# Kernel tuning notes

Measured on AMD Instinct MI355X. Metric: run time of the kernel, lower is better.

Reference implementation:

```python
import jax, jax.numpy as jnp
import numpy as np

S = 72
IMG_W, IMG_H = 640, 360
STRIDE = 32
FMAP_H, FMAP_W = IMG_H // STRIDE, IMG_W // STRIDE  # 11, 20
N_OFFSETS = S
N_STRIPS = S - 1
ANGLES = np.array([15.0, 22.0, 30.0, 39.0, 49.0, 60.0, 72.0, 80.0, 90.0, 100.0, 108.0, 120.0, 131.0, 141.0, 150.0, 158.0, 165.0])
N_ANG = 17
N_PRED = 2 + 2 + 1 + N_OFFSETS  # 77
N_EDGE = FMAP_W + 2 * FMAP_H    # 42
N_PROP = N_ANG * N_EDGE         # 714
NMS_THRES = 15.0
BACKBONE_C = 512
CONV_C = 1024


def _make_anchors():
    anchor_ys = np.linspace(1.0, 0.0, N_OFFSETS)
    tan = np.tan(np.deg2rad(ANGLES))
    def side(origins):
        out = np.zeros((N_ANG, N_PRED, len(origins)), np.float32)
        for i, (sx, sy) in enumerate(origins):
            out[:, 2, i] = 1.0 - sy
            out[:, 3, i] = sx
            out[:, 5:, i] = (sx + (sy - anchor_ys)[None, :] / tan[:, None]) * IMG_W
        return out.reshape(N_ANG * N_PRED, len(origins))
    left = side([(0.0, y) for y in np.linspace(1.0, 0.0, FMAP_H)])
    right = side([(1.0, y) for y in np.linspace(1.0, 0.0, FMAP_H)])
    bottom = side([(x, 1.0) for x in np.linspace(1.0, 0.0, FMAP_W)])
    anchors = np.zeros((N_ANG * N_PRED, FMAP_H, FMAP_W), np.float32)
    anchors[:, :, 0] = left
    anchors[:, :, -1] = right
    anchors[:, -1, :] = bottom
    edge = np.concatenate([anchors[:, :, 0], anchors[:, :, -1], anchors[:, -1, :]], 1)  # [1309,42]
    anch_dim = edge.reshape(N_ANG, N_PRED, N_EDGE).transpose(2, 0, 1).reshape(N_PROP, N_PRED)
    return jnp.asarray(anchors), jnp.asarray(anch_dim)


def setup_inputs():
    key = jax.random.key(0)
    ks = jax.random.split(key, 4)
    B = 32
    feat = jax.random.normal(ks[0], (B, BACKBONE_C, FMAP_H, FMAP_W), jnp.float32)
    W_conv = jax.random.normal(ks[1], (CONV_C, BACKBONE_C), jnp.float32) * 0.02
    b_conv = jnp.zeros((CONV_C,), jnp.float32)
    W_cls = jax.random.normal(ks[2], (2 * N_ANG, CONV_C), jnp.float32) * 0.02
    b_cls = jnp.zeros((2 * N_ANG,), jnp.float32)
    W_reg = jax.random.normal(ks[3], (N_ANG * (N_OFFSETS + 1), CONV_C), jnp.float32) * 0.02
    b_reg = jnp.zeros((N_ANG * (N_OFFSETS + 1),), jnp.float32)
    anchors, anchors_anchor_dim = _make_anchors()
    return {"feat": feat, "W_conv": W_conv, "b_conv": b_conv, "W_cls": W_cls, "b_cls": b_cls,
            "W_reg": W_reg, "b_reg": b_reg, "anchors": anchors, "anchors_anchor_dim": anchors_anchor_dim}


def _proposals(feat, W_conv, b_conv, W_cls, b_cls, W_reg, b_reg, anchors):
    B = feat.shape[0]
    features = jnp.einsum('bchw,oc->bohw', feat, W_conv) + b_conv[None, :, None, None]
    cls_f = jnp.einsum('bchw,oc->bohw', features, W_cls) + b_cls[None, :, None, None]
    reg_f = jnp.einsum('bchw,oc->bohw', features, W_reg) + b_reg[None, :, None, None]
    anch = anchors.reshape(N_ANG, N_PRED, FMAP_H, FMAP_W)
    cls_r = cls_f.reshape(B, N_ANG, 2, FMAP_H, FMAP_W)
    reg_r = reg_f.reshape(B, N_ANG, N_OFFSETS + 1, FMAP_H, FMAP_W)
    # slots 0:2 <- cls logits (set), slots 2:4 <- anchor (copied), slots 4: <- anchor + reg
    mid = jnp.broadcast_to(anch[None, :, 2:4], (B, N_ANG, 2, FMAP_H, FMAP_W))
    tail = anch[None, :, 4:] + reg_r
    lane = jnp.concatenate([cls_r, mid, tail], axis=2)  # [B,17,77,h,w]
    # gather the three feature-map edges: left col, right col, bottom row
    edges = jnp.concatenate([lane[:, :, :, :, 0], lane[:, :, :, :, -1], lane[:, :, :, -1, :]], axis=3)  # [B,17,77,42]
    return edges.transpose(0, 3, 1, 2).reshape(B, N_PROP, N_PRED)  # [B,714,77]


def _nms_one(props, scores):
    # greedy line-NMS over proposals of one image, shapes static
    order = jnp.argsort(-scores)
    p = props[order]
    start = jnp.clip(jnp.round(p[:, 2] * N_STRIPS), 0.0, float(N_STRIPS))
    end = jnp.clip(start + p[:, 4] - 1.0, 0.0, float(N_STRIPS))
    xs = p[:, 5:]  # [N,72]
    s = jnp.maximum(start[:, None], start[None, :])
    e = jnp.minimum(end[:, None], end[None, :])
    idx = jnp.arange(N_OFFSETS, dtype=p.dtype)
    m = (idx[None, None, :] >= s[..., None]) & (idx[None, None, :] <= e[..., None])  # [N,N,72]
    diff = jnp.abs(xs[:, None, :] - xs[None, :, :])  # [N,N,72]
    cnt = e - s + 1.0
    dist = jnp.where(cnt > 0, jnp.sum(diff * m, -1) / jnp.maximum(cnt, 1.0), jnp.inf)
    sup = dist < NMS_THRES
    n = p.shape[0]
    pos = jnp.arange(n)
    def step(suppressed, i):
        keep_i = ~suppressed[i]
        suppressed = suppressed | (keep_i & sup[i] & (pos > i))
        return suppressed, keep_i
    _, keep_sorted = jax.lax.scan(step, jnp.zeros(n, bool), pos)
    return jnp.zeros(n, bool).at[order].set(keep_sorted)


def reference(feat, W_conv, b_conv, W_cls, b_cls, W_reg, b_reg, anchors, anchors_anchor_dim):
    proposals = _proposals(feat, W_conv, b_conv, W_cls, b_cls, W_reg, b_reg, anchors)
    scores = jax.nn.softmax(proposals[..., :2], axis=-1)[..., 1]  # [B,714]
    keep_mask = jax.lax.map(lambda pr: _nms_one(pr[0], pr[1]), (proposals, scores))  # [B,714]
    return proposals, keep_mask, scores
```

## Files before the change

kernel.cpp:

```cpp
#include <hip/hip_runtime.h>
#include <math.h>

#define NB     32
#define FH     11
#define FW     20
#define CIN    512
#define CMID   1024
#define NANG   17
#define NPREDD 77
#define NEDGE  42
#define NPROPP 714
#define NOFF   72
#define NCLS   34
#define NREGR  1241
#define N2PAD  1280
#define MTOT   1344
#define NSTRIPSF 71.0f
#define PADK   40

typedef unsigned long long u64;
typedef unsigned short ushortt;
typedef short s8v __attribute__((ext_vector_type(8)));
typedef float f4v __attribute__((ext_vector_type(4)));

__device__ inline ushortt f2bf(float f) {
    unsigned u = __float_as_uint(f);
    u += 0x7fffu + ((u >> 16) & 1u);
    return (ushortt)(u >> 16);
}
__device__ inline float bf2f(ushortt h) {
    return __uint_as_float(((unsigned)h) << 16);
}

__global__ __launch_bounds__(256) void k_gather_split(const float* __restrict__ feat,
                                                      ushortt* __restrict__ Ahi,
                                                      ushortt* __restrict__ Alo)
{
    int idx = blockIdx.x * 256 + threadIdx.x;
    int m = idx >> 9, c = idx & 511;
    int b = m / NEDGE, e = m - b * NEDGE;
    int h, w;
    if (e < FH)          { h = e;      w = 0;      }
    else if (e < 2 * FH) { h = e - FH; w = FW - 1; }
    else                 { h = FH - 1; w = e - 2 * FH; }
    float v = feat[((size_t)(b * CIN + c) * FH + h) * FW + w];
    ushortt hi = f2bf(v);
    Ahi[idx] = hi;
    Alo[idx] = f2bf(v - bf2f(hi));
}

__global__ __launch_bounds__(256) void k_gemm1m(const ushortt* __restrict__ Ahi,
                                                const ushortt* __restrict__ Alo,
                                                const float* __restrict__ W,
                                                const float* __restrict__ bias,
                                                ushortt* __restrict__ Chi,
                                                ushortt* __restrict__ Clo)
{
    const int K = CIN, N = CMID;
    __shared__ __align__(16) ushortt Ash[64 * PADK], Asl[64 * PADK];
    __shared__ __align__(16) ushortt Bsh[64 * PADK], Bsl[64 * PADK];
    int tid = threadIdx.x;
    int m0 = blockIdx.y * 64, n0 = blockIdx.x * 64;
    int srow = tid >> 2, sg = tid & 3;
    int lane = tid & 63, wv = tid >> 6;
    int wm = (wv & 1) * 32, wn = (wv >> 1) * 32;
    int quad = lane >> 4, l15 = lane & 15;

    f4v acc[2][2];
#pragma unroll
    for (int i = 0; i < 2; ++i)
#pragma unroll
        for (int j = 0; j < 2; ++j) acc[i][j] = (f4v){0.f, 0.f, 0.f, 0.f};

    const ushortt* Ahp = Ahi + (size_t)(m0 + srow) * K + sg * 8;
    const ushortt* Alp = Alo + (size_t)(m0 + srow) * K + sg * 8;
    const float*   Wp  = W   + (size_t)(n0 + srow) * K + sg * 8;

    for (int k0 = 0; k0 < K; k0 += 32) {
        __syncthreads();
        s8v av = *(const s8v*)(Ahp + k0);
        s8v lv = *(const s8v*)(Alp + k0);
        float4 w0 = *(const float4*)(Wp + k0);
        float4 w1 = *(const float4*)(Wp + k0 + 4);
        float wf[8] = {w0.x, w0.y, w0.z, w0.w, w1.x, w1.y, w1.z, w1.w};
        s8v wh, wl;
#pragma unroll
        for (int j = 0; j < 8; ++j) {
            ushortt h = f2bf(wf[j]);
            wh[j] = (short)h;
            wl[j] = (short)f2bf(wf[j] - bf2f(h));
        }
        *(s8v*)&Ash[srow * PADK + sg * 8] = av;
        *(s8v*)&Asl[srow * PADK + sg * 8] = lv;
        *(s8v*)&Bsh[srow * PADK + sg * 8] = wh;
        *(s8v*)&Bsl[srow * PADK + sg * 8] = wl;
        __syncthreads();
        s8v ah[2], al[2], bh[2], bl[2];
#pragma unroll
        for (int s = 0; s < 2; ++s) {
            ah[s] = *(const s8v*)&Ash[(wm + s * 16 + l15) * PADK + quad * 8];
            al[s] = *(const s8v*)&Asl[(wm + s * 16 + l15) * PADK + quad * 8];
            bh[s] = *(const s8v*)&Bsh[(wn + s * 16 + l15) * PADK + quad * 8];
            bl[s] = *(const s8v*)&Bsl[(wn + s * 16 + l15) * PADK + quad * 8];
        }
#pragma unroll
        for (int sm = 0; sm < 2; ++sm)
#pragma unroll
            for (int sn = 0; sn < 2; ++sn) {
                acc[sm][sn] = __builtin_amdgcn_mfma_f32_16x16x32_bf16(al[sm], bl[sn], acc[sm][sn], 0, 0, 0);
                acc[sm][sn] = __builtin_amdgcn_mfma_f32_16x16x32_bf16(al[sm], bh[sn], acc[sm][sn], 0, 0, 0);
                acc[sm][sn] = __builtin_amdgcn_mfma_f32_16x16x32_bf16(ah[sm], bl[sn], acc[sm][sn], 0, 0, 0);
                acc[sm][sn] = __builtin_amdgcn_mfma_f32_16x16x32_bf16(ah[sm], bh[sn], acc[sm][sn], 0, 0, 0);
            }
    }
#pragma unroll
    for (int sm = 0; sm < 2; ++sm)
#pragma unroll
        for (int sn = 0; sn < 2; ++sn)
#pragma unroll
            for (int r = 0; r < 4; ++r) {
                int m = m0 + wm + sm * 16 + quad * 4 + r;
                int n = n0 + wn + sn * 16 + l15;
                float v = acc[sm][sn][r] + bias[n];
                ushortt h = f2bf(v);
                Chi[(size_t)m * N + n] = h;
                Clo[(size_t)m * N + n] = f2bf(v - bf2f(h));
            }
}

__global__ __launch_bounds__(256) void k_gemm2m(const ushortt* __restrict__ Ahi,
                                                const ushortt* __restrict__ Alo,
                                                const float* __restrict__ Wcls,
                                                const float* __restrict__ bcls,
                                                const float* __restrict__ Wreg,
                                                const float* __restrict__ breg,
                                                float* __restrict__ C)
{
    const int K = CMID;
    __shared__ __align__(16) ushortt Ash[64 * PADK], Asl[64 * PADK];
    __shared__ __align__(16) ushortt Bsh[64 * PADK], Bsl[64 * PADK];
    int tid = threadIdx.x;
    int m0 = blockIdx.y * 64, n0 = blockIdx.x * 64;
    int srow = tid >> 2, sg = tid & 3;
    int lane = tid & 63, wv = tid >> 6;
    int wm = (wv & 1) * 32, wn = (wv >> 1) * 32;
    int quad = lane >> 4, l15 = lane & 15;

    f4v acc[2][2];
#pragma unroll
    for (int i = 0; i < 2; ++i)
#pragma unroll
        for (int j = 0; j < 2; ++j) acc[i][j] = (f4v){0.f, 0.f, 0.f, 0.f};

    const ushortt* Ahp = Ahi + (size_t)(m0 + srow) * K + sg * 8;
    const ushortt* Alp = Alo + (size_t)(m0 + srow) * K + sg * 8;
    int nrow = n0 + srow;
    const float* Wp = Wcls;
    bool wvalid = true;
    if (nrow < NCLS)              Wp = Wcls + (size_t)nrow * K + sg * 8;
    else if (nrow < NCLS + NREGR) Wp = Wreg + (size_t)(nrow - NCLS) * K + sg * 8;
    else                          wvalid = false;

    for (int k0 = 0; k0 < K; k0 += 32) {
        __syncthreads();
        s8v av = *(const s8v*)(Ahp + k0);
        s8v lv = *(const s8v*)(Alp + k0);
        float4 w0, w1;
        if (wvalid) {
            w0 = *(const float4*)(Wp + k0);
            w1 = *(const float4*)(Wp + k0 + 4);
        } else {
            w0 = make_float4(0.f, 0.f, 0.f, 0.f);
            w1 = w0;
        }
        float wf[8] = {w0.x, w0.y, w0.z, w0.w, w1.x, w1.y, w1.z, w1.w};
        s8v wh, wl;
#pragma unroll
        for (int j = 0; j < 8; ++j) {
            ushortt h = f2bf(wf[j]);
            wh[j] = (short)h;
            wl[j] = (short)f2bf(wf[j] - bf2f(h));
        }
        *(s8v*)&Ash[srow * PADK + sg * 8] = av;
        *(s8v*)&Asl[srow * PADK + sg * 8] = lv;
        *(s8v*)&Bsh[srow * PADK + sg * 8] = wh;
        *(s8v*)&Bsl[srow * PADK + sg * 8] = wl;
        __syncthreads();
        s8v ah[2], al[2], bh[2], bl[2];
#pragma unroll
        for (int s = 0; s < 2; ++s) {
            ah[s] = *(const s8v*)&Ash[(wm + s * 16 + l15) * PADK + quad * 8];
            al[s] = *(const s8v*)&Asl[(wm + s * 16 + l15) * PADK + quad * 8];
            bh[s] = *(const s8v*)&Bsh[(wn + s * 16 + l15) * PADK + quad * 8];
            bl[s] = *(const s8v*)&Bsl[(wn + s * 16 + l15) * PADK + quad * 8];
        }
#pragma unroll
        for (int sm = 0; sm < 2; ++sm)
#pragma unroll
            for (int sn = 0; sn < 2; ++sn) {
                acc[sm][sn] = __builtin_amdgcn_mfma_f32_16x16x32_bf16(al[sm], bl[sn], acc[sm][sn], 0, 0, 0);
                acc[sm][sn] = __builtin_amdgcn_mfma_f32_16x16x32_bf16(al[sm], bh[sn], acc[sm][sn], 0, 0, 0);
                acc[sm][sn] = __builtin_amdgcn_mfma_f32_16x16x32_bf16(ah[sm], bl[sn], acc[sm][sn], 0, 0, 0);
                acc[sm][sn] = __builtin_amdgcn_mfma_f32_16x16x32_bf16(ah[sm], bh[sn], acc[sm][sn], 0, 0, 0);
            }
    }
#pragma unroll
    for (int sm = 0; sm < 2; ++sm)
#pragma unroll
        for (int sn = 0; sn < 2; ++sn)
#pragma unroll
            for (int r = 0; r < 4; ++r) {
                int m = m0 + wm + sm * 16 + quad * 4 + r;
                int n = n0 + wn + sn * 16 + l15;
                float bb = (n < NCLS) ? bcls[n] : ((n < NCLS + NREGR) ? breg[n - NCLS] : 0.f);
                C[(size_t)m * N2PAD + n] = acc[sm][sn][r] + bb;
            }
}

__global__ __launch_bounds__(256) void k_assemble(const float* __restrict__ C2,
                                                  const float* __restrict__ AD,
                                                  float* __restrict__ outP,
                                                  float* __restrict__ outS,
                                                  float* __restrict__ startv,
                                                  float* __restrict__ endv,
                                                  float* __restrict__ xsel)
{
    int mb = blockIdx.x;
    int b = mb / NEDGE, e = mb - b * NEDGE;
    const float* c2 = C2 + (size_t)mb * N2PAD;
    int tid = threadIdx.x;
    for (int idx = tid; idx < NANG * NPREDD; idx += 256) {
        int a = idx / NPREDD, p = idx - a * NPREDD;
        int prop = e * NANG + a;
        float v;
        if (p < 2) v = c2[a * 2 + p];
        else {
            v = AD[prop * NPREDD + p];
            if (p >= 4) v += c2[NCLS + a * 73 + (p - 4)];
        }
        outP[((size_t)b * NPROPP + prop) * NPREDD + p] = v;
    }
    if (tid < NANG) {
        int a = tid, prop = e * NANG + a;
        float c0 = c2[2 * a], c1 = c2[2 * a + 1];
        float mx = fmaxf(c0, c1);
        float e0 = expf(c0 - mx), e1 = expf(c1 - mx);
        outS[b * NPROPP + prop] = e1 / (e0 + e1);
        float p2 = AD[prop * NPREDD + 2];
        float p4 = AD[prop * NPREDD + 4] + c2[NCLS + a * 73];
        float st = fminf(fmaxf(rintf(p2 * NSTRIPSF), 0.0f), NSTRIPSF);
        float en = fminf(fmaxf(st + p4 - 1.0f, 0.0f), NSTRIPSF);
        startv[b * 720 + prop] = st;
        endv[b * 720 + prop] = en;
        int ksi = (int)st;
        xsel[b * 720 + prop] = AD[prop * NPREDD + 5 + ksi] + c2[NCLS + a * 73 + ksi + 1];
    }
}

__global__ __launch_bounds__(128) void k_sort(const float* __restrict__ scores,
                                              int* __restrict__ order)
{
    int b = blockIdx.x, tile = blockIdx.y, tid = threadIdx.x;
    __shared__ __align__(16) float s[720];
    for (int x = tid; x < 720; x += 128)
        s[x] = (x < NPROPP) ? scores[b * NPROPP + x] : -1e30f;
    __syncthreads();
    int i = tile * 128 + tid;
    if (i >= NPROPP) return;
    float si = s[i];
    int r = 0;
#pragma unroll 4
    for (int j4 = 0; j4 < 720; j4 += 4) {
        float4 v = *(const float4*)&s[j4];
        r += (v.x > si) || (v.x == si && (j4 + 0) < i);
        r += (v.y > si) || (v.y == si && (j4 + 1) < i);
        r += (v.z > si) || (v.z == si && (j4 + 2) < i);
        r += (v.w > si) || (v.w == si && (j4 + 3) < i);
    }
    order[b * 720 + r] = i;
}

__global__ __launch_bounds__(256) void k_supmat(const float* __restrict__ outP,
                                                const float* __restrict__ startv,
                                                const float* __restrict__ endv,
                                                const float* __restrict__ xsel,
                                                const int* __restrict__ order,
                                                u64* __restrict__ sup)
{
    int jt = blockIdx.x, it = blockIdx.y, b = blockIdx.z;
    int i0 = it * 64, j0 = jt * 64;
    int tid = threadIdx.x;
    if (j0 + 63 < i0) {
        if (tid < 64) {
            int il = i0 + tid;
            if (il < NPROPP) sup[((size_t)b * NPROPP + il) * 12 + jt] = 0ull;
        }
        return;
    }
    __shared__ float SI[64], EI[64], XI[64];
    __shared__ float SJ[64], EJ[64], XJ[64];
    __shared__ int   OI[64], OJ[64];
    if (tid < 128) {
        int side = tid >> 6, q = tid & 63;
        int pos = (side ? j0 : i0) + q;
        int o = (pos < NPROPP) ? order[b * 720 + pos] : -1;
        float st = (o >= 0) ? startv[b * 720 + o] : 0.f;
        float en = (o >= 0) ? endv[b * 720 + o] : -2.f;
        float xv = (o >= 0) ? xsel[b * 720 + o] : 0.f;
        if (!side) { SI[q] = st; EI[q] = en; XI[q] = xv; OI[q] = o; }
        else       { SJ[q] = st; EJ[q] = en; XJ[q] = xv; OJ[q] = o; }
    }
    __syncthreads();
    int lane = tid & 63, w = tid >> 6;
    int j = j0 + lane;
    float sj = SJ[lane], ej = EJ[lane], xj = XJ[lane];
    const float* basexs = outP + (size_t)b * NPROPP * NPREDD + 5;
#pragma unroll 1
    for (int rep = 0; rep < 16; ++rep) {
        int iloc = w * 16 + rep;
        int il = i0 + iloc;
        float si = SI[iloc], ei = EI[iloc];
        float s = fmaxf(si, sj), e = fminf(ei, ej);
        float cnt = e - s + 1.0f;
        bool sp = false;
        if (cnt > 0.f) {
            if (e < s) {
                sp = true;
            } else {
                int ks = (int)s, ke = (int)e;
                if (si == sj && ke == ks) {
                    sp = (fabsf(XI[iloc] - xj) / fmaxf(cnt, 1.0f)) < 15.0f;
                } else {
                    const float* xi  = basexs + (size_t)OI[iloc] * NPREDD;
                    const float* xjp = basexs + (size_t)OJ[lane] * NPREDD;
                    float sum = 0.f;
                    for (int k = ks; k <= ke; ++k)
                        sum += fabsf(xi[k] - xjp[k]);
                    sp = (sum / fmaxf(cnt, 1.0f)) < 15.0f;
                }
            }
        }
        bool valid = (il < NPROPP) && (j < NPROPP) && (j > il);
        u64 msk = __ballot(valid && sp);
        if (lane == 0 && il < NPROPP)
            sup[((size_t)b * NPROPP + il) * 12 + jt] = msk;
    }
}

__global__ __launch_bounds__(64) void k_scan(const u64* __restrict__ sup,
                                             const int* __restrict__ order,
                                             float* __restrict__ keep_out)
{
    int b = blockIdx.x, lane = threadIdx.x;
    __shared__ float keepv[NPROPP];
    __shared__ int ord[NPROPP];
    for (int x = lane; x < NPROPP; x += 64) { keepv[x] = 0.f; ord[x] = order[b * 720 + x]; }
    __syncthreads();
    const u64* base = sup + (size_t)b * NPROPP * 12;

    u64 P[12];
#pragma unroll
    for (int t = 0; t < 12; ++t) P[t] = 0ull;

    u64 cur[12], nxt[12];
    {
        int r = lane;
#pragma unroll
        for (int t = 0; t < 12; ++t)
            cur[t] = (r < NPROPP) ? base[(size_t)r * 12 + t] : 0ull;
    }

#pragma unroll
    for (int c = 0; c < 12; ++c) {
        if (c < 11) {
            int r = (c + 1) * 64 + lane;
#pragma unroll
            for (int t = 0; t < 12; ++t) {
                int w = c + 1 + t;
                nxt[t] = (r < NPROPP && w < 12) ? base[(size_t)r * 12 + w] : 0ull;
            }
        }
        unsigned plo = (unsigned)P[c], phi = (unsigned)(P[c] >> 32);
#pragma unroll
        for (int s = 1; s < 64; s <<= 1) {
            plo |= __shfl_xor(plo, s, 64);
            phi |= __shfl_xor(phi, s, 64);
        }
        u64 S0 = ((u64)phi << 32) | (u64)plo;
        u64 c0 = cur[0];
        u64 keepbits = 0ull;
#pragma unroll
        for (int ib = 0; ib < 64; ++ib) {
            u64 row = ((u64)(unsigned)__builtin_amdgcn_readlane((int)(c0 >> 32), ib) << 32)
                    |  (u64)(unsigned)__builtin_amdgcn_readlane((int)(unsigned)c0, ib);
            u64 m = ((S0 >> ib) & 1ull) - 1ull;
            S0 |= row & m;
            keepbits |= m & (1ull << ib);
        }
        int imax = NPROPP - c * 64; if (imax > 64) imax = 64;
        if (lane < imax)
            keepv[ord[c * 64 + lane]] = ((keepbits >> lane) & 1ull) ? 1.f : 0.f;
        u64 lm = 0ull - ((keepbits >> lane) & 1ull);
#pragma unroll
        for (int t = 1; t < 12; ++t)
            if (c + t < 12) P[c + t] |= cur[t] & lm;
#pragma unroll
        for (int t = 0; t < 12; ++t) cur[t] = nxt[t];
    }
    __syncthreads();
    for (int x = lane; x < NPROPP; x += 64) keep_out[b * NPROPP + x] = keepv[x];
}

extern "C" void kernel_launch(void* const* d_in, const int* in_sizes, int n_in,
                              void* d_out, int out_size, void* d_ws, size_t ws_size,
                              hipStream_t stream)
{
    const float* feat  = (const float*)d_in[0];
    const float* Wconv = (const float*)d_in[1];
    const float* bconv = (const float*)d_in[2];
    const float* Wcls  = (const float*)d_in[3];
    const float* bcls  = (const float*)d_in[4];
    const float* Wreg  = (const float*)d_in[5];
    const float* breg  = (const float*)d_in[6];
    const float* AD    = (const float*)d_in[8];

    float* out  = (float*)d_out;
    float* outP = out;
    float* outK = out + (size_t)NB * NPROPP * NPREDD;
    float* outS = outK + (size_t)NB * NPROPP;

    float* ws = (float*)d_ws;
    ushortt* A1hi = (ushortt*)ws;
    ushortt* A1lo = (ushortt*)(ws + 344064);
    ushortt* A2hi = (ushortt*)(ws + 688128);
    ushortt* A2lo = (ushortt*)(ws + 1376256);
    float*   C2   = ws + 2064384;
    float* startv = ws;
    float* endv   = ws + 23040;
    int*   order  = (int*)(ws + 46080);
    u64*   sup    = (u64*)(ws + 69120);
    float* xsel   = ws + 617472;

    k_gather_split<<<dim3(2688),       dim3(256), 0, stream>>>(feat, A1hi, A1lo);
    k_gemm1m      <<<dim3(16, 21),     dim3(256), 0, stream>>>(A1hi, A1lo, Wconv, bconv, A2hi, A2lo);
    k_gemm2m      <<<dim3(20, 21),     dim3(256), 0, stream>>>(A2hi, A2lo, Wcls, bcls, Wreg, breg, C2);
    k_assemble    <<<dim3(MTOT),       dim3(256), 0, stream>>>(C2, AD, outP, outS, startv, endv, xsel);
    k_sort        <<<dim3(NB, 6),      dim3(128), 0, stream>>>(outS, order);
    k_supmat      <<<dim3(12, 12, NB), dim3(256), 0, stream>>>(outP, startv, endv, xsel, order, sup);
    k_scan        <<<dim3(NB),         dim3(64),  0, stream>>>(sup, order, outK);
}
```

Before: 208.6 us.

## Replace sequential greedy NMS scan with parallel fixed-point sweeps

The NMS keep computation no longer walks proposals one by one with wave-level readlane steps. It now holds all suppression rows in registers across 256 threads. Each sweep recomputes the keep set as valid proposals not suppressed by any currently kept proposal, ORing across lanes and waves through shuffles and shared-memory atomics, until nothing changes. Because the matrix is upper-triangular this reaches the greedy result, but the number of sweeps depends on suppression chain depth. Each sweep costs many shuffles and two block barriers, so deep chains could be slower than the old serial scan.

```diff
diff --git a/kernel.cpp b/kernel.cpp
--- a/kernel.cpp
+++ b/kernel.cpp
@@ -347,68 +347,75 @@
     }
 }
 
-__global__ __launch_bounds__(64) void k_scan(const u64* __restrict__ sup,
-                                             const int* __restrict__ order,
-                                             float* __restrict__ keep_out)
-{
-    int b = blockIdx.x, lane = threadIdx.x;
-    __shared__ float keepv[NPROPP];
-    __shared__ int ord[NPROPP];
-    for (int x = lane; x < NPROPP; x += 64) { keepv[x] = 0.f; ord[x] = order[b * 720 + x]; }
+__global__ __launch_bounds__(256) void k_scan(const u64* __restrict__ sup,
+                                              const int* __restrict__ order,
+                                              float* __restrict__ keep_out)
+{
+    int b = blockIdx.x, tid = threadIdx.x;
+    int lane = tid & 63;
+    __shared__ u64 K[12], NS[12];
+    __shared__ int changed;
+    const u64* base = sup + (size_t)b * NPROPP * 12;
+
+    int r0 = tid, r1 = tid + 256, r2 = tid + 512;
+    u64 row0[12], row1[12], row2[12];
+#pragma unroll
+    for (int t = 0; t < 12; ++t) {
+        row0[t] = base[(size_t)r0 * 12 + t];
+        row1[t] = (r1 < NPROPP) ? base[(size_t)r1 * 12 + t] : 0ull;
+        row2[t] = (r2 < NPROPP) ? base[(size_t)r2 * 12 + t] : 0ull;
+    }
+    if (tid < 12) {
+        K[tid] = (tid < 11) ? ~0ull : ((1ull << (NPROPP - 704)) - 1ull);
+        NS[tid] = 0ull;
+    }
     __syncthreads();
-    const u64* base = sup + (size_t)b * NPROPP * 12;
-
-    u64 P[12];
-#pragma unroll
-    for (int t = 0; t < 12; ++t) P[t] = 0ull;
-
-    u64 cur[12], nxt[12];
-    {
-        int r = lane;
-#pragma unroll
-        for (int t = 0; t < 12; ++t)
-            cur[t] = (r < NPROPP) ? base[(size_t)r * 12 + t] : 0ull;
-    }
-
-#pragma unroll
-    for (int c = 0; c < 12; ++c) {
-        if (c < 11) {
-            int r = (c + 1) * 64 + lane;
+
+    for (int sweep = 0; sweep < 720; ++sweep) {
+        u64 m0 = 0ull - ((K[r0 >> 6] >> (r0 & 63)) & 1ull);
+        u64 m1 = (r1 < NPROPP) ? (0ull - ((K[r1 >> 6] >> (r1 & 63)) & 1ull)) : 0ull;
+        u64 m2 = (r2 < NPROPP) ? (0ull - ((K[r2 >> 6] >> (r2 & 63)) & 1ull)) : 0ull;
+        unsigned lo[12], hi[12];
+#pragma unroll
+        for (int t = 0; t < 12; ++t) {
+            u64 a = (row0[t] & m0) | (row1[t] & m1) | (row2[t] & m2);
+            lo[t] = (unsigned)a;
+            hi[t] = (unsigned)(a >> 32);
+        }
+#pragma unroll
+        for (int s = 1; s < 64; s <<= 1) {
 #pragma unroll
             for (int t = 0; t < 12; ++t) {
-                int w = c + 1 + t;
-                nxt[t] = (r < NPROPP && w < 12) ? base[(size_t)r * 12 + w] : 0ull;
-            }
-        }
-        unsigned plo = (unsigned)P[c], phi = (unsigned)(P[c] >> 32);
-#pragma unroll
-        for (int s = 1; s < 64; s <<= 1) {
-            plo |= __shfl_xor(plo, s, 64);
-            phi |= __shfl_xor(phi, s, 64);
-        }
-        u64 S0 = ((u64)phi << 32) | (u64)plo;
-        u64 c0 = cur[0];
-        u64 keepbits = 0ull;
-#pragma unroll
-        for (int ib = 0; ib < 64; ++ib) {
-            u64 row = ((u64)(unsigned)__builtin_amdgcn_readlane((int)(c0 >> 32), ib) << 32)
-                    |  (u64)(unsigned)__builtin_amdgcn_readlane((int)(unsigned)c0, ib);
-            u64 m = ((S0 >> ib) & 1ull) - 1ull;
-            S0 |= row & m;
-            keepbits |= m & (1ull << ib);
-        }
-        int imax = NPROPP - c * 64; if (imax > 64) imax = 64;
-        if (lane < imax)
-            keepv[ord[c * 64 + lane]] = ((keepbits >> lane) & 1ull) ? 1.f : 0.f;
-        u64 lm = 0ull - ((keepbits >> lane) & 1ull);
-#pragma unroll
-        for (int t = 1; t < 12; ++t)
-            if (c + t < 12) P[c + t] |= cur[t] & lm;
-#pragma unroll
-        for (int t = 0; t < 12; ++t) cur[t] = nxt[t];
-    }
-    __syncthreads();
-    for (int x = lane; x < NPROPP; x += 64) keep_out[b * NPROPP + x] = keepv[x];
+                lo[t] |= __shfl_xor(lo[t], s, 64);
+                hi[t] |= __shfl_xor(hi[t], s, 64);
+            }
+        }
+        if (tid == 0) changed = 0;
+        if (lane == 0) {
+#pragma unroll
+            for (int t = 0; t < 12; ++t)
+                atomicOr(&NS[t], ((u64)hi[t] << 32) | (u64)lo[t]);
+        }
+        __syncthreads();
+        if (tid < 12) {
+            u64 valid = (tid < 11) ? ~0ull : ((1ull << (NPROPP - 704)) - 1ull);
+            u64 nk = valid & ~NS[tid];
+            if (nk != K[tid]) changed = 1;
+            K[tid] = nk;
+            NS[tid] = 0ull;
+        }
+        __syncthreads();
+        if (!changed) break;
+    }
+    if (r0 < NPROPP)
+        keep_out[b * NPROPP + order[b * 720 + r0]] =
+            ((K[r0 >> 6] >> (r0 & 63)) & 1ull) ? 1.f : 0.f;
+    if (r1 < NPROPP)
+        keep_out[b * NPROPP + order[b * 720 + r1]] =
+            ((K[r1 >> 6] >> (r1 & 63)) & 1ull) ? 1.f : 0.f;
+    if (r2 < NPROPP)
+        keep_out[b * NPROPP + order[b * 720 + r2]] =
+            ((K[r2 >> 6] >> (r2 & 63)) & 1ull) ? 1.f : 0.f;
 }
 
 extern "C" void kernel_launch(void* const* d_in, const int* in_sizes, int n_in,
@@ -447,5 +454,5 @@
     k_assemble    <<<dim3(MTOT),       dim3(256), 0, stream>>>(C2, AD, outP, outS, startv, endv, xsel);
     k_sort        <<<dim3(NB, 6),      dim3(128), 0, stream>>>(outS, order);
     k_supmat      <<<dim3(12, 12, NB), dim3(256), 0, stream>>>(outP, startv, endv, xsel, order, sup);
-    k_scan        <<<dim3(NB),         dim3(64),  0, stream>>>(sup, order, outK);
-}
+    k_scan        <<<dim3(NB),         dim3(256), 0, stream>>>(sup, order, outK);
+}
```

Result: faster. 192.4 us, median of 2 (-7.8%).
